# Kernel tuning notes

Measured on AMD Instinct MI355X. Metric: run time of the kernel, lower is better.

The kernel has to match this reference:

```python
import jax, jax.numpy as jnp
import numpy as np

B, S, D, H = 4, 2048, 1024, 16
NEG = -1e10  # matches the module's -10000000000.0 additive mask


def setup_inputs() -> dict:
    key = jax.random.key(0)
    k1, k2, k3, k4, k5 = jax.random.split(key, 5)
    scale = 0.02
    return {
        "x": jax.random.normal(k1, (B, S, D), dtype=jnp.float32),
        "w_qkv": jax.random.normal(k2, (D, 3 * D), dtype=jnp.float32) * scale,
        "b_qkv": jax.random.normal(k3, (3 * D,), dtype=jnp.float32) * scale,
        "w_out": jax.random.normal(k4, (D, D), dtype=jnp.float32) * scale,
        "b_out": jax.random.normal(k5, (D,), dtype=jnp.float32) * scale,
    }


def reference(x, w_qkv, b_qkv, w_out, b_out):
    b, s, d = x.shape
    hd = d // H  # per-head dim
    qkv = x @ w_qkv + b_qkv  # [b,s,3d]
    qq, kk, vv = jnp.split(qkv, 3, axis=-1)
    # [b,h,s,hd]
    qq = qq.reshape(b, s, H, hd).transpose(0, 2, 1, 3)
    kk = kk.reshape(b, s, H, hd).transpose(0, 2, 1, 3)
    vv = vv.reshape(b, s, H, hd).transpose(0, 2, 1, 3)
    scale = 1.0 / float(hd) ** 0.5
    # additive causal mask: NEG above diagonal, 0 on/below (as in module)
    mask = (1.0 - jnp.tri(s, dtype=jnp.float32)) * NEG
    attn = jnp.einsum("bhqd,bhkd->bhqk", qq, kk) * scale + mask
    attn = jax.nn.softmax(attn, axis=-1)
    out = jnp.einsum("bhqk,bhkd->bhqd", attn, vv)  # [b,h,s,hd]
    out = out.transpose(0, 2, 1, 3).reshape(b, s, d)
    return out @ w_out + b_out
```

## Files before the change

### kernel.cpp

```cpp
#include <hip/hip_runtime.h>
#include <hip/hip_bf16.h>
#include <stdint.h>
#include <type_traits>


#define B_   4
#define S_   2048
#define D_   1024
#define H_   16
#define HD_  64
#define MTOK (B_ * S_)
#define BK   32
#define QSCALE 0.18033688011112042f

typedef __attribute__((ext_vector_type(8))) short bfx8;
typedef __attribute__((ext_vector_type(4))) float fx4;
typedef __attribute__((ext_vector_type(16))) float fx16;

#define MAX3(a,b,c) fmaxf(fmaxf(a,b),c)

static __device__ __forceinline__ unsigned short f2bf(float f) {
    union { float f; uint32_t u; } v{f};
    uint32_t u = v.u;
    u += 0x7fffu + ((u >> 16) & 1u);
    return (unsigned short)(u >> 16);
}

static __device__ __forceinline__ uint32_t cvtpk(float lo, float hi) {
    uint32_t r;
    asm volatile("v_cvt_pk_bf16_f32 %0, %1, %2" : "=v"(r) : "v"(lo), "v"(hi));
    return r;
}

static __device__ __forceinline__ void pswap(uint32_t& a, uint32_t& b) {
    asm volatile("v_permlane32_swap_b32 %0, %1" : "+v"(a), "+v"(b));
}

static __device__ __forceinline__ void gll16(const unsigned short* g, const unsigned short* l) {
    typedef const __attribute__((address_space(1))) void* gp_t;
    typedef __attribute__((address_space(3))) void* lp_t;
    __builtin_amdgcn_global_load_lds((gp_t)(uintptr_t)g, (lp_t)(uint32_t)(uintptr_t)l, 16, 0, 0);
}

__global__ void k_conv_x(const float* __restrict__ x, unsigned short* __restrict__ xb, int n8) {
    int i = blockIdx.x * blockDim.x + threadIdx.x;
    int stride = gridDim.x * blockDim.x;
    for (; i < n8; i += stride) {
        const float4* p = (const float4*)(x + (size_t)i * 8);
        float4 a = p[0], b = p[1];
        bfx8 o;
        o[0]=f2bf(a.x); o[1]=f2bf(a.y); o[2]=f2bf(a.z); o[3]=f2bf(a.w);
        o[4]=f2bf(b.x); o[5]=f2bf(b.y); o[6]=f2bf(b.z); o[7]=f2bf(b.w);
        *(bfx8*)(xb + (size_t)i * 8) = o;
    }
}

__global__ void k_transpose_bf(const float* __restrict__ w, unsigned short* __restrict__ wt,
                               int K, int N) {
    int idx = blockIdx.x * blockDim.x + threadIdx.x;
    int total = N * (K / 8);
    if (idx >= total) return;
    int n  = idx % N;
    int k0 = (idx / N) * 8;
    bfx8 o;
#pragma unroll
    for (int j = 0; j < 8; ++j) o[j] = f2bf(w[(size_t)(k0 + j) * N + n]);
    *(bfx8*)(wt + (size_t)n * K + k0) = o;
}

__global__ void k_transpose_v(const unsigned short* __restrict__ Vw,
                              unsigned short* __restrict__ Vt) {
    __shared__ unsigned short lds[64][72];
    const int bg = blockIdx.x;
    const int bh = bg >> 5;
    const int st = (bg & 31) * 64;
    const int t = threadIdx.x;
#pragma unroll
    for (int j = 0; j < 2; ++j) {
        int c = t + 256 * j;
        int row = c >> 3, q = c & 7;
        *(bfx8*)&lds[row][q * 8] = *(const bfx8*)&Vw[((size_t)bh * S_ + st + row) * HD_ + q * 8];
    }
    __syncthreads();
#pragma unroll
    for (int j = 0; j < 2; ++j) {
        int c = t + 256 * j;
        int d = c >> 3, q = c & 7;
        bfx8 o;
#pragma unroll
        for (int e = 0; e < 8; ++e) o[e] = lds[q * 8 + e][d];
        *(bfx8*)&Vt[((size_t)bh * HD_ + d) * S_ + st + q * 8] = o;
    }
}

__launch_bounds__(256)
__global__ void k_gemm_qkv(const unsigned short* __restrict__ A,
                           const unsigned short* __restrict__ Bt,
                           const float* __restrict__ bias,
                           unsigned short* __restrict__ Qw,
                           unsigned short* __restrict__ Kw,
                           unsigned short* __restrict__ Vw) {
    __shared__ unsigned short Al[2][128 * BK];
    __shared__ unsigned short Bl[2][128 * BK];
    const int wg = blockIdx.x;
    const int lin = (wg & 7) * 192 + (wg >> 3);
    const int ny = lin / 24, nx = lin - ny * 24;
    const int m0 = ny * 128;
    const int n0 = nx * 128;
    const int t = threadIdx.x;
    const int w = t >> 6, l = t & 63;
    const int wr = w >> 1, wc = w & 1;
    const int lr = l & 15, lg = l >> 4;
    const int srow = l >> 2;
    const int scol = (l & 3) * 8;
    fx4 acc[4][4] = {};

    auto stage = [&](int k0, int buf) {
#pragma unroll
        for (int j = 0; j < 2; ++j) {
            int rb = j * 64 + w * 16;
            gll16(&A [(size_t)(m0 + rb + srow) * D_ + k0 + scol], &Al[buf][rb * BK]);
            gll16(&Bt[(size_t)(n0 + rb + srow) * D_ + k0 + scol], &Bl[buf][rb * BK]);
        }
    };
    auto compute = [&](auto bufc) {
        constexpr int BUF = decltype(bufc)::value;
        bfx8 af[4], bf[4];
#pragma unroll
        for (int i = 0; i < 4; ++i) af[i] = *(const bfx8*)&Al[BUF][(wr * 64 + i * 16 + lr) * BK + lg * 8];
#pragma unroll
        for (int i = 0; i < 4; ++i) bf[i] = *(const bfx8*)&Bl[BUF][(wc * 64 + i * 16 + lr) * BK + lg * 8];
#pragma unroll
        for (int mi = 0; mi < 4; ++mi)
#pragma unroll
            for (int ni = 0; ni < 4; ++ni)
                acc[mi][ni] = __builtin_amdgcn_mfma_f32_16x16x32_bf16(bf[ni], af[mi], acc[mi][ni], 0, 0, 0);
    };

    stage(0, 0);
    __syncthreads();
    for (int k0 = 0; k0 < D_; k0 += 2 * BK) {
        if (k0 + BK < D_) stage(k0 + BK, 1);
        compute(std::integral_constant<int, 0>{});
        __syncthreads();
        if (k0 + 2 * BK < D_) stage(k0 + 2 * BK, 0);
        compute(std::integral_constant<int, 1>{});
        __syncthreads();
    }

#pragma unroll
    for (int ni = 0; ni < 4; ++ni) {
        const int nn = n0 + wc * 64 + ni * 16 + lg * 4;
        const int mat = nn >> 10;
        const int h = (nn & 1023) >> 6, dd = nn & 63;
        const float4 bv = *(const float4*)&bias[nn];
        unsigned short* dst = (mat == 0) ? Qw : (mat == 1) ? Kw : Vw;
        const float sc = (mat == 0) ? QSCALE : 1.0f;
#pragma unroll
        for (int mi = 0; mi < 4; ++mi) {
            const int m = m0 + wr * 64 + mi * 16 + lr;
            const int b = m >> 11, s = m & 2047;
            const int bh = b * H_ + h;
            fx4 v = acc[mi][ni];
            float o0 = (v[0] + bv.x) * sc, o1 = (v[1] + bv.y) * sc;
            float o2 = (v[2] + bv.z) * sc, o3 = (v[3] + bv.w) * sc;
            uint2 u; u.x = cvtpk(o0, o1); u.y = cvtpk(o2, o3);
            *(uint2*)&dst[((size_t)bh * S_ + s) * HD_ + dd] = u;
        }
    }
}

__launch_bounds__(512, 4)
__global__ void k_attn(const unsigned short* __restrict__ Qw,
                       const unsigned short* __restrict__ Kw,
                       const unsigned short* __restrict__ Vt,
                       unsigned short* __restrict__ Ob) {
    __shared__ unsigned short Sh[4][64 * 64];
    const int wg = blockIdx.x;
    const int xcd = wg & 7, ix = wg >> 3;
    const int bh = xcd * 8 + (ix >> 3);
    const int pi = ix & 7;
    const int t = threadIdx.x;
    const int w = t >> 6, l = t & 63;
    const int lq = l & 31, hi = l >> 5;
    const int tile = (w < 4) ? (15 - pi) : pi;
    const int qr = tile * 128 + (w & 3) * 32;
    const int NT = 32 - 2 * pi;

    const unsigned short* Qp = Qw + (size_t)bh * S_ * HD_;
    const unsigned short* Kp = Kw + (size_t)bh * S_ * HD_;
    const unsigned short* Vp = Vt + (size_t)bh * HD_ * S_;

    bfx8 qf[4];
#pragma unroll
    for (int kb = 0; kb < 4; ++kb)
        qf[kb] = *(const bfx8*)&Qp[(size_t)(qr + lq) * HD_ + kb * 16 + hi * 8];

    fx16 oacc[2] = {};
    float mrow = -1e30f, lsum = 0.f;

    const int sid0 = t, sid1 = t + 512;
    const int srow0 = (sid0 & 511) >> 3, sq0 = sid0 & 7;
    const int srow1 = (sid1 & 511) >> 3, sq1 = sid1 & 7;
    const int soff0 = srow0 * 128 + ((sq0 * 16) ^ ((srow0 & 7) << 4));
    const int soff1 = srow1 * 128 + ((sq1 * 16) ^ ((srow1 & 7) << 4));

    auto step = [&](auto bufc, int tkv) {
        constexpr int BUF = decltype(bufc)::value;
        const int kv0 = tkv * 64;
        const bool pre = (tkv + 1 < NT);
        bfx8 sreg0, sreg1;
        if (pre) {
            const int kn = kv0 + 64;
            sreg0 = *(const bfx8*)&Kp[(size_t)(kn + srow0) * HD_ + sq0 * 8];
            sreg1 = *(const bfx8*)&Vp[(size_t)srow1 * S_ + kn + sq1 * 8];
        }
        if (kv0 <= qr + 31) {
            const char* Kb = (const char*)&Sh[BUF][0];
            const char* Vb = (const char*)&Sh[2 + BUF][0];
            const int sw = (lq & 7) << 4;
            fx16 s0 = {}, s1 = {};
            __builtin_amdgcn_s_setprio(1);
#pragma unroll
            for (int kb = 0; kb < 4; ++kb) {
                const int cb = kb * 32 + hi * 16;
                bfx8 k0 = *(const bfx8*)(Kb + lq * 128 + (cb ^ sw));
                bfx8 k1 = *(const bfx8*)(Kb + (32 + lq) * 128 + (cb ^ sw));
                s0 = __builtin_amdgcn_mfma_f32_32x32x16_bf16(k0, qf[kb], s0, 0, 0, 0);
                s1 = __builtin_amdgcn_mfma_f32_32x32x16_bf16(k1, qf[kb], s1, 0, 0, 0);
            }
            __builtin_amdgcn_s_setprio(0);
            if (kv0 + 63 > qr) {
                const int qrel = qr + lq - kv0;
#pragma unroll
                for (int r = 0; r < 16; ++r) {
                    const int kvo = (r & 3) + 8 * (r >> 2) + 4 * hi;
                    if (kvo > qrel)      s0[r] = -1e30f;
                    if (kvo + 32 > qrel) s1[r] = -1e30f;
                }
            }
            float a0 = MAX3(s0[0], s0[1], s0[2]);
            float a1 = MAX3(s0[3], s0[4], s0[5]);
            float a2 = MAX3(s0[6], s0[7], s0[8]);
            float a3 = MAX3(s0[9], s0[10], s0[11]);
            float a4 = MAX3(s0[12], s0[13], s0[14]);
            float a5 = MAX3(s0[15], s1[0], s1[1]);
            float a6 = MAX3(s1[2], s1[3], s1[4]);
            float a7 = MAX3(s1[5], s1[6], s1[7]);
            float a8 = MAX3(s1[8], s1[9], s1[10]);
            float a9 = MAX3(s1[11], s1[12], s1[13]);
            float aA = fmaxf(s1[14], s1[15]);
            float b0 = MAX3(a0, a1, a2);
            float b1 = MAX3(a3, a4, a5);
            float b2 = MAX3(a6, a7, a8);
            float b3 = fmaxf(a9, aA);
            float mx = MAX3(fmaxf(b0, b1), b2, b3);
            mx = fmaxf(mx, __shfl_xor(mx, 32));
            if (!__all(mx <= mrow + 8.f)) {
                const float mnew = fmaxf(mrow, mx);
                const float al = exp2f(mrow - mnew);
                mrow = mnew;
#pragma unroll
                for (int r = 0; r < 16; ++r) { oacc[0][r] *= al; oacc[1][r] *= al; }
                lsum *= al;
            }
            uint32_t pk0[8], pk1[8];
            float ps = 0.f;
#pragma unroll
            for (int j = 0; j < 8; ++j) {
                float p0 = exp2f(s0[2 * j] - mrow), p1 = exp2f(s0[2 * j + 1] - mrow);
                float p2 = exp2f(s1[2 * j] - mrow), p3 = exp2f(s1[2 * j + 1] - mrow);
                ps += (p0 + p1) + (p2 + p3);
                pk0[j] = cvtpk(p0, p1);
                pk1[j] = cvtpk(p2, p3);
            }
            lsum += ps + __shfl_xor(ps, 32);
            __builtin_amdgcn_s_setprio(1);
#pragma unroll
            for (int sl = 0; sl < 4; ++sl) {
                const uint32_t* pk = (sl < 2) ? pk0 : pk1;
                const int s = sl & 1;
                uint32_t w0 = pk[4 * s], w1 = pk[4 * s + 1], w2 = pk[4 * s + 2], w3 = pk[4 * s + 3];
                pswap(w0, w2);
                pswap(w1, w3);
                union { uint32_t u[4]; bfx8 v; } pf;
                pf.u[0] = w0; pf.u[1] = w1; pf.u[2] = w2; pf.u[3] = w3;
                const int cb = sl * 32 + hi * 16;
                bfx8 v0 = *(const bfx8*)(Vb + lq * 128 + (cb ^ sw));
                bfx8 v1 = *(const bfx8*)(Vb + (32 + lq) * 128 + (cb ^ sw));
                oacc[0] = __builtin_amdgcn_mfma_f32_32x32x16_bf16(v0, pf.v, oacc[0], 0, 0, 0);
                oacc[1] = __builtin_amdgcn_mfma_f32_32x32x16_bf16(v1, pf.v, oacc[1], 0, 0, 0);
            }
            __builtin_amdgcn_s_setprio(0);
        }
        if (pre) {
            *(bfx8*)((char*)&Sh[BUF ^ 1][0] + soff0) = sreg0;
            *(bfx8*)((char*)&Sh[2 + (BUF ^ 1)][0] + soff1) = sreg1;
        }
    };

    {
        bfx8 s0 = *(const bfx8*)&Kp[(size_t)srow0 * HD_ + sq0 * 8];
        bfx8 s1 = *(const bfx8*)&Vp[(size_t)srow1 * S_ + sq1 * 8];
        *(bfx8*)((char*)&Sh[0][0] + soff0) = s0;
        *(bfx8*)((char*)&Sh[2][0] + soff1) = s1;
    }
    __syncthreads();

    for (int tkv = 0; tkv < NT; tkv += 2) {
        step(std::integral_constant<int, 0>{}, tkv);
        __syncthreads();
        step(std::integral_constant<int, 1>{}, tkv + 1);
        __syncthreads();
    }

    const int b = bh >> 4, h = bh & 15;
    const float iv = __builtin_amdgcn_rcpf(lsum);
    unsigned short* orow = Ob + ((size_t)b * S_ + qr + lq) * D_ + h * 64;
#pragma unroll
    for (int db = 0; db < 2; ++db)
#pragma unroll
        for (int rq = 0; rq < 4; ++rq) {
            uint2 u;
            u.x = cvtpk(oacc[db][rq * 4 + 0] * iv, oacc[db][rq * 4 + 1] * iv);
            u.y = cvtpk(oacc[db][rq * 4 + 2] * iv, oacc[db][rq * 4 + 3] * iv);
            *(uint2*)&orow[db * 32 + rq * 8 + hi * 4] = u;
        }
}

__launch_bounds__(256)
__global__ void k_gemm_proj(const unsigned short* __restrict__ A,
                            const unsigned short* __restrict__ Bt,
                            const float* __restrict__ bias,
                            float* __restrict__ out) {
    __shared__ unsigned short Al[2][128 * BK];
    __shared__ unsigned short Bl[2][128 * BK];
    const int wg = blockIdx.x;
    const int lin = (wg & 7) * 64 + (wg >> 3);
    const int ny = lin >> 3, nx = lin & 7;
    const int m0 = ny * 128;
    const int n0 = nx * 128;
    const int t = threadIdx.x;
    const int w = t >> 6, l = t & 63;
    const int wr = w >> 1, wc = w & 1;
    const int lr = l & 15, lg = l >> 4;
    const int srow = l >> 2;
    const int scol = (l & 3) * 8;
    fx4 acc[4][4] = {};

    auto stage = [&](int k0, int buf) {
#pragma unroll
        for (int j = 0; j < 2; ++j) {
            int rb = j * 64 + w * 16;
            gll16(&A [(size_t)(m0 + rb + srow) * D_ + k0 + scol], &Al[buf][rb * BK]);
            gll16(&Bt[(size_t)(n0 + rb + srow) * D_ + k0 + scol], &Bl[buf][rb * BK]);
        }
    };
    auto compute = [&](auto bufc) {
        constexpr int BUF = decltype(bufc)::value;
        bfx8 af[4], bf[4];
#pragma unroll
        for (int i = 0; i < 4; ++i) af[i] = *(const bfx8*)&Al[BUF][(wr * 64 + i * 16 + lr) * BK + lg * 8];
#pragma unroll
        for (int i = 0; i < 4; ++i) bf[i] = *(const bfx8*)&Bl[BUF][(wc * 64 + i * 16 + lr) * BK + lg * 8];
#pragma unroll
        for (int mi = 0; mi < 4; ++mi)
#pragma unroll
            for (int ni = 0; ni < 4; ++ni)
                acc[mi][ni] = __builtin_amdgcn_mfma_f32_16x16x32_bf16(bf[ni], af[mi], acc[mi][ni], 0, 0, 0);
    };

    stage(0, 0);
    __syncthreads();
    for (int k0 = 0; k0 < D_; k0 += 2 * BK) {
        if (k0 + BK < D_) stage(k0 + BK, 1);
        compute(std::integral_constant<int, 0>{});
        __syncthreads();
        if (k0 + 2 * BK < D_) stage(k0 + 2 * BK, 0);
        compute(std::integral_constant<int, 1>{});
        __syncthreads();
    }
#pragma unroll
    for (int ni = 0; ni < 4; ++ni) {
        const int nn = n0 + wc * 64 + ni * 16 + lg * 4;
        const float4 bv = *(const float4*)&bias[nn];
#pragma unroll
        for (int mi = 0; mi < 4; ++mi) {
            const int m = m0 + wr * 64 + mi * 16 + lr;
            fx4 v = acc[mi][ni];
            float4 o; o.x = v[0] + bv.x; o.y = v[1] + bv.y; o.z = v[2] + bv.z; o.w = v[3] + bv.w;
            *(float4*)&out[(size_t)m * D_ + nn] = o;
        }
    }
}

extern "C" void kernel_launch(void* const* d_in, const int* in_sizes, int n_in,
                              void* d_out, int out_size, void* d_ws, size_t ws_size,
                              hipStream_t stream) {
    const float* x     = (const float*)d_in[0];
    const float* w_qkv = (const float*)d_in[1];
    const float* b_qkv = (const float*)d_in[2];
    const float* w_out = (const float*)d_in[3];
    const float* b_out = (const float*)d_in[4];
    float* out = (float*)d_out;

    unsigned short* xb    = (unsigned short*)d_ws;
    unsigned short* wqkvT = xb    + (size_t)MTOK * D_;
    unsigned short* woutT = wqkvT + (size_t)3 * D_ * D_;
    unsigned short* Qw    = woutT + (size_t)D_ * D_;
    unsigned short* Kw    = Qw    + (size_t)MTOK * D_;
    unsigned short* Vw    = Kw    + (size_t)MTOK * D_;
    unsigned short* attnb = Vw    + (size_t)MTOK * D_;
    unsigned short* Vt    = xb;

    k_conv_x<<<2048, 256, 0, stream>>>(x, xb, MTOK * D_ / 8);
    k_transpose_bf<<<(3 * D_ * (D_ / 8)) / 256, 256, 0, stream>>>(w_qkv, wqkvT, D_, 3 * D_);
    k_transpose_bf<<<(D_ * (D_ / 8)) / 256, 256, 0, stream>>>(w_out, woutT, D_, D_);
    k_gemm_qkv<<<1536, 256, 0, stream>>>(xb, wqkvT, b_qkv, Qw, Kw, Vw);
    k_transpose_v<<<2048, 256, 0, stream>>>(Vw, Vt);
    k_attn<<<512, 512, 0, stream>>>(Qw, Kw, Vt, attnb);
    k_gemm_proj<<<512, 256, 0, stream>>>(attnb, woutT, b_out, out);
}
```

Before: 204.8 us.

## Rewrite QKV GEMM with 256x256 tiles, swizzled LDS and interleaved staging

The QKV projection GEMM moves from 128x128 tiles with BK=32 and 256 threads to 256x256 tiles with BK=64 and 512 threads (8 waves, each computing 128x64). LDS rows are XOR-swizzled to avoid bank conflicts. Global-to-LDS prefetch of the next k-tile is split into four quarters interleaved between MFMA quadrants, using explicit vmcnt waits, barriers and setprio. The aim is higher arithmetic intensity and better overlap of loads with MFMA, at the cost of more registers and LDS per block and only 384 blocks to fill the CUs.

```diff
diff --git a/kernel.cpp b/kernel.cpp
--- a/kernel.cpp
+++ b/kernel.cpp
@@ -11,6 +11,8 @@
 #define HD_  64
 #define MTOK (B_ * S_)
 #define BK   32
+#define QBM  256
+#define QBK  64
 #define QSCALE 0.18033688011112042f
 
 typedef __attribute__((ext_vector_type(8))) short bfx8;
@@ -93,78 +95,129 @@
     }
 }
 
-__launch_bounds__(256)
+__launch_bounds__(512, 2)
 __global__ void k_gemm_qkv(const unsigned short* __restrict__ A,
                            const unsigned short* __restrict__ Bt,
                            const float* __restrict__ bias,
                            unsigned short* __restrict__ Qw,
                            unsigned short* __restrict__ Kw,
                            unsigned short* __restrict__ Vw) {
-    __shared__ unsigned short Al[2][128 * BK];
-    __shared__ unsigned short Bl[2][128 * BK];
+    __shared__ unsigned short Al[2][QBM * QBK];
+    __shared__ unsigned short Bl[2][QBM * QBK];
     const int wg = blockIdx.x;
-    const int lin = (wg & 7) * 192 + (wg >> 3);
-    const int ny = lin / 24, nx = lin - ny * 24;
-    const int m0 = ny * 128;
-    const int n0 = nx * 128;
+    const int lin = (wg & 7) * 48 + (wg >> 3);
+    const int ny = lin / 12, nx = lin - ny * 12;
+    const int m0 = ny * QBM, n0 = nx * QBM;
     const int t = threadIdx.x;
     const int w = t >> 6, l = t & 63;
-    const int wr = w >> 1, wc = w & 1;
+    const int wr = w >> 2, wc = w & 3;
     const int lr = l & 15, lg = l >> 4;
-    const int srow = l >> 2;
-    const int scol = (l & 3) * 8;
-    fx4 acc[4][4] = {};
-
-    auto stage = [&](int k0, int buf) {
+    const int sw = (lr & 7) << 4;
+
+    fx4 acc[8][4] = {};
+    bfx8 afH[4][2], bf0[2][2], bf1[2][2];
+
+    const int g_r  = l >> 3;
+    const int g_cb = ((l & 7) * 16) ^ (g_r << 4);
+
+    auto stage_half = [&](int buf, int kt1, int half) {
+        const int k0 = kt1 * QBK;
+        const int gr0 = (half >> 1) * 128;
 #pragma unroll
         for (int j = 0; j < 2; ++j) {
-            int rb = j * 64 + w * 16;
-            gll16(&A [(size_t)(m0 + rb + srow) * D_ + k0 + scol], &Al[buf][rb * BK]);
-            gll16(&Bt[(size_t)(n0 + rb + srow) * D_ + k0 + scol], &Bl[buf][rb * BK]);
-        }
-    };
-    auto compute = [&](auto bufc) {
-        constexpr int BUF = decltype(bufc)::value;
-        bfx8 af[4], bf[4];
-#pragma unroll
-        for (int i = 0; i < 4; ++i) af[i] = *(const bfx8*)&Al[BUF][(wr * 64 + i * 16 + lr) * BK + lg * 8];
-#pragma unroll
-        for (int i = 0; i < 4; ++i) bf[i] = *(const bfx8*)&Bl[BUF][(wc * 64 + i * 16 + lr) * BK + lg * 8];
+            const int rbase = gr0 + j * 64 + w * 8;
+            const int grow = rbase + g_r;
+            if (half & 1)
+                gll16(&Bt[(size_t)(n0 + grow) * D_ + k0] + (g_cb >> 1), &Bl[buf][rbase * QBK]);
+            else
+                gll16(&A [(size_t)(m0 + grow) * D_ + k0] + (g_cb >> 1), &Al[buf][rbase * QBK]);
+        }
+    };
+
+    auto loadA = [&](const unsigned short* base, int mh) {
+        const char* p = (const char*)base;
+#pragma unroll
+        for (int mi = 0; mi < 4; ++mi) {
+            const int row = wr * 128 + mh * 64 + mi * 16 + lr;
+#pragma unroll
+            for (int kk = 0; kk < 2; ++kk)
+                afH[mi][kk] = *(const bfx8*)(p + row * 128 + ((kk * 64 + lg * 16) ^ sw));
+        }
+    };
+    auto loadB = [&](const unsigned short* base, int nh, bfx8 (*bf)[2]) {
+        const char* p = (const char*)base;
+#pragma unroll
+        for (int ni = 0; ni < 2; ++ni) {
+            const int row = wc * 64 + nh * 32 + ni * 16 + lr;
+#pragma unroll
+            for (int kk = 0; kk < 2; ++kk)
+                bf[ni][kk] = *(const bfx8*)(p + row * 128 + ((kk * 64 + lg * 16) ^ sw));
+        }
+    };
+    auto quad = [&](int mh, int nh, bfx8 (*bf)[2]) {
+        __builtin_amdgcn_s_setprio(1);
 #pragma unroll
         for (int mi = 0; mi < 4; ++mi)
 #pragma unroll
-            for (int ni = 0; ni < 4; ++ni)
-                acc[mi][ni] = __builtin_amdgcn_mfma_f32_16x16x32_bf16(bf[ni], af[mi], acc[mi][ni], 0, 0, 0);
-    };
-
-    stage(0, 0);
-    __syncthreads();
-    for (int k0 = 0; k0 < D_; k0 += 2 * BK) {
-        if (k0 + BK < D_) stage(k0 + BK, 1);
-        compute(std::integral_constant<int, 0>{});
-        __syncthreads();
-        if (k0 + 2 * BK < D_) stage(k0 + 2 * BK, 0);
-        compute(std::integral_constant<int, 1>{});
-        __syncthreads();
-    }
-
+            for (int ni = 0; ni < 2; ++ni)
+#pragma unroll
+                for (int kk = 0; kk < 2; ++kk)
+                    acc[mh * 4 + mi][nh * 2 + ni] = __builtin_amdgcn_mfma_f32_16x16x32_bf16(
+                        bf[ni][kk], afH[mi][kk], acc[mh * 4 + mi][nh * 2 + ni], 0, 0, 0);
+        __builtin_amdgcn_s_setprio(0);
+    };
+
+    stage_half(0, 0, 0); stage_half(0, 0, 1); stage_half(0, 0, 2); stage_half(0, 0, 3);
+
+    const int NKT = D_ / QBK;
+    for (int kt = 0; kt < NKT; ++kt) {
+        const int cur = kt & 1, nxt = cur ^ 1;
+        const bool pre = (kt + 1 < NKT);
+        if (pre) {
+            stage_half(nxt, kt + 1, 0);
+            asm volatile("s_waitcnt vmcnt(2)" ::: "memory");
+        } else {
+            asm volatile("s_waitcnt vmcnt(0)" ::: "memory");
+        }
+        __builtin_amdgcn_sched_barrier(0);
+        __builtin_amdgcn_s_barrier();
+        loadA(&Al[cur][0], 0);
+        loadB(&Bl[cur][0], 0, bf0);
+        quad(0, 0, bf0);
+        __builtin_amdgcn_s_barrier();
+        loadB(&Bl[cur][0], 1, bf1);
+        if (pre) stage_half(nxt, kt + 1, 1);
+        __builtin_amdgcn_s_barrier();
+        quad(0, 1, bf1);
+        __builtin_amdgcn_s_barrier();
+        loadA(&Al[cur][0], 1);
+        if (pre) stage_half(nxt, kt + 1, 2);
+        __builtin_amdgcn_s_barrier();
+        quad(1, 1, bf1);
+        __builtin_amdgcn_s_barrier();
+        if (pre) stage_half(nxt, kt + 1, 3);
+        __builtin_amdgcn_s_barrier();
+        quad(1, 0, bf0);
+        __builtin_amdgcn_s_barrier();
+    }
+
+    const int mat = n0 >> 10;
+    unsigned short* dst = (mat == 0) ? Qw : (mat == 1) ? Kw : Vw;
+    const float sc = (mat == 0) ? QSCALE : 1.0f;
 #pragma unroll
     for (int ni = 0; ni < 4; ++ni) {
         const int nn = n0 + wc * 64 + ni * 16 + lg * 4;
-        const int mat = nn >> 10;
         const int h = (nn & 1023) >> 6, dd = nn & 63;
         const float4 bv = *(const float4*)&bias[nn];
-        unsigned short* dst = (mat == 0) ? Qw : (mat == 1) ? Kw : Vw;
-        const float sc = (mat == 0) ? QSCALE : 1.0f;
-#pragma unroll
-        for (int mi = 0; mi < 4; ++mi) {
-            const int m = m0 + wr * 64 + mi * 16 + lr;
+#pragma unroll
+        for (int mi = 0; mi < 8; ++mi) {
+            const int m = m0 + wr * 128 + mi * 16 + lr;
             const int b = m >> 11, s = m & 2047;
             const int bh = b * H_ + h;
             fx4 v = acc[mi][ni];
-            float o0 = (v[0] + bv.x) * sc, o1 = (v[1] + bv.y) * sc;
-            float o2 = (v[2] + bv.z) * sc, o3 = (v[3] + bv.w) * sc;
-            uint2 u; u.x = cvtpk(o0, o1); u.y = cvtpk(o2, o3);
+            uint2 u;
+            u.x = cvtpk((v[0] + bv.x) * sc, (v[1] + bv.y) * sc);
+            u.y = cvtpk((v[2] + bv.z) * sc, (v[3] + bv.w) * sc);
             *(uint2*)&dst[((size_t)bh * S_ + s) * HD_ + dd] = u;
         }
     }
@@ -416,7 +469,7 @@
     k_conv_x<<<2048, 256, 0, stream>>>(x, xb, MTOK * D_ / 8);
     k_transpose_bf<<<(3 * D_ * (D_ / 8)) / 256, 256, 0, stream>>>(w_qkv, wqkvT, D_, 3 * D_);
     k_transpose_bf<<<(D_ * (D_ / 8)) / 256, 256, 0, stream>>>(w_out, woutT, D_, D_);
-    k_gemm_qkv<<<1536, 256, 0, stream>>>(xb, wqkvT, b_qkv, Qw, Kw, Vw);
+    k_gemm_qkv<<<384, 512, 0, stream>>>(xb, wqkvT, b_qkv, Qw, Kw, Vw);
     k_transpose_v<<<2048, 256, 0, stream>>>(Vw, Vt);
     k_attn<<<512, 512, 0, stream>>>(Qw, Kw, Vt, attnb);
     k_gemm_proj<<<512, 256, 0, stream>>>(attnb, woutT, b_out, out);
```

Result: faster. 198.1 us (-3.3%).

## Split attention into 256-thread single-tile blocks and drop QKV GEMM double buffering

Applied to the files above, without the earlier changes.

The attention kernel drops its paired heavy/light causal tiles in 512-thread blocks and launches 1024 blocks of 256 threads, each covering one 128-row query tile. Blocks are ordered heaviest first, and each thread now stages two K and two V chunks. Separately, the QKV GEMM loses its double-buffered LDS pipeline and becomes single-buffered with two barriers per K step, halving LDS use. The GEMM change exposes global-load latency. The attention change gives up the explicit load balancing, which now depends on scheduling order.

```diff
diff --git a/kernel.cpp b/kernel.cpp
--- a/kernel.cpp
+++ b/kernel.cpp
@@ -100,8 +100,8 @@
                            unsigned short* __restrict__ Qw,
                            unsigned short* __restrict__ Kw,
                            unsigned short* __restrict__ Vw) {
-    __shared__ unsigned short Al[2][128 * BK];
-    __shared__ unsigned short Bl[2][128 * BK];
+    __shared__ unsigned short Al[128 * BK];
+    __shared__ unsigned short Bl[128 * BK];
     const int wg = blockIdx.x;
     const int lin = (wg & 7) * 192 + (wg >> 3);
     const int ny = lin / 24, nx = lin - ny * 24;
@@ -115,37 +115,25 @@
     const int scol = (l & 3) * 8;
     fx4 acc[4][4] = {};
 
-    auto stage = [&](int k0, int buf) {
+    for (int k0 = 0; k0 < D_; k0 += BK) {
+        __syncthreads();
 #pragma unroll
         for (int j = 0; j < 2; ++j) {
             int rb = j * 64 + w * 16;
-            gll16(&A [(size_t)(m0 + rb + srow) * D_ + k0 + scol], &Al[buf][rb * BK]);
-            gll16(&Bt[(size_t)(n0 + rb + srow) * D_ + k0 + scol], &Bl[buf][rb * BK]);
-        }
-    };
-    auto compute = [&](auto bufc) {
-        constexpr int BUF = decltype(bufc)::value;
+            gll16(&A [(size_t)(m0 + rb + srow) * D_ + k0 + scol], &Al[rb * BK]);
+            gll16(&Bt[(size_t)(n0 + rb + srow) * D_ + k0 + scol], &Bl[rb * BK]);
+        }
+        __syncthreads();
         bfx8 af[4], bf[4];
 #pragma unroll
-        for (int i = 0; i < 4; ++i) af[i] = *(const bfx8*)&Al[BUF][(wr * 64 + i * 16 + lr) * BK + lg * 8];
-#pragma unroll
-        for (int i = 0; i < 4; ++i) bf[i] = *(const bfx8*)&Bl[BUF][(wc * 64 + i * 16 + lr) * BK + lg * 8];
+        for (int i = 0; i < 4; ++i) af[i] = *(const bfx8*)&Al[(wr * 64 + i * 16 + lr) * BK + lg * 8];
+#pragma unroll
+        for (int i = 0; i < 4; ++i) bf[i] = *(const bfx8*)&Bl[(wc * 64 + i * 16 + lr) * BK + lg * 8];
 #pragma unroll
         for (int mi = 0; mi < 4; ++mi)
 #pragma unroll
             for (int ni = 0; ni < 4; ++ni)
                 acc[mi][ni] = __builtin_amdgcn_mfma_f32_16x16x32_bf16(bf[ni], af[mi], acc[mi][ni], 0, 0, 0);
-    };
-
-    stage(0, 0);
-    __syncthreads();
-    for (int k0 = 0; k0 < D_; k0 += 2 * BK) {
-        if (k0 + BK < D_) stage(k0 + BK, 1);
-        compute(std::integral_constant<int, 0>{});
-        __syncthreads();
-        if (k0 + 2 * BK < D_) stage(k0 + 2 * BK, 0);
-        compute(std::integral_constant<int, 1>{});
-        __syncthreads();
     }
 
 #pragma unroll
@@ -170,7 +158,7 @@
     }
 }
 
-__launch_bounds__(512, 4)
+__launch_bounds__(256, 4)
 __global__ void k_attn(const unsigned short* __restrict__ Qw,
                        const unsigned short* __restrict__ Kw,
                        const unsigned short* __restrict__ Vt,
@@ -178,14 +166,13 @@
     __shared__ unsigned short Sh[4][64 * 64];
     const int wg = blockIdx.x;
     const int xcd = wg & 7, ix = wg >> 3;
-    const int bh = xcd * 8 + (ix >> 3);
-    const int pi = ix & 7;
+    const int bh = xcd * 8 + (ix >> 4);
+    const int ti = 15 - (ix & 15);
     const int t = threadIdx.x;
     const int w = t >> 6, l = t & 63;
     const int lq = l & 31, hi = l >> 5;
-    const int tile = (w < 4) ? (15 - pi) : pi;
-    const int qr = tile * 128 + (w & 3) * 32;
-    const int NT = 32 - 2 * pi;
+    const int qr = ti * 128 + w * 32;
+    const int NT = 2 * ti + 2;
 
     const unsigned short* Qp = Qw + (size_t)bh * S_ * HD_;
     const unsigned short* Kp = Kw + (size_t)bh * S_ * HD_;
@@ -199,21 +186,22 @@
     fx16 oacc[2] = {};
     float mrow = -1e30f, lsum = 0.f;
 
-    const int sid0 = t, sid1 = t + 512;
-    const int srow0 = (sid0 & 511) >> 3, sq0 = sid0 & 7;
-    const int srow1 = (sid1 & 511) >> 3, sq1 = sid1 & 7;
-    const int soff0 = srow0 * 128 + ((sq0 * 16) ^ ((srow0 & 7) << 4));
-    const int soff1 = srow1 * 128 + ((sq1 * 16) ^ ((srow1 & 7) << 4));
+    const int sr0 = t >> 3,         sq0 = t & 7;
+    const int sr1 = (t + 256) >> 3, sq1 = (t + 256) & 7;
+    const int so0 = sr0 * 128 + ((sq0 * 16) ^ ((sr0 & 7) << 4));
+    const int so1 = sr1 * 128 + ((sq1 * 16) ^ ((sr1 & 7) << 4));
 
     auto step = [&](auto bufc, int tkv) {
         constexpr int BUF = decltype(bufc)::value;
         const int kv0 = tkv * 64;
         const bool pre = (tkv + 1 < NT);
-        bfx8 sreg0, sreg1;
+        bfx8 sK0, sK1, sV0, sV1;
         if (pre) {
             const int kn = kv0 + 64;
-            sreg0 = *(const bfx8*)&Kp[(size_t)(kn + srow0) * HD_ + sq0 * 8];
-            sreg1 = *(const bfx8*)&Vp[(size_t)srow1 * S_ + kn + sq1 * 8];
+            sK0 = *(const bfx8*)&Kp[(size_t)(kn + sr0) * HD_ + sq0 * 8];
+            sK1 = *(const bfx8*)&Kp[(size_t)(kn + sr1) * HD_ + sq1 * 8];
+            sV0 = *(const bfx8*)&Vp[(size_t)sr0 * S_ + kn + sq0 * 8];
+            sV1 = *(const bfx8*)&Vp[(size_t)sr1 * S_ + kn + sq1 * 8];
         }
         if (kv0 <= qr + 31) {
             const char* Kb = (const char*)&Sh[BUF][0];
@@ -294,16 +282,22 @@
             __builtin_amdgcn_s_setprio(0);
         }
         if (pre) {
-            *(bfx8*)((char*)&Sh[BUF ^ 1][0] + soff0) = sreg0;
-            *(bfx8*)((char*)&Sh[2 + (BUF ^ 1)][0] + soff1) = sreg1;
+            *(bfx8*)((char*)&Sh[BUF ^ 1][0] + so0) = sK0;
+            *(bfx8*)((char*)&Sh[BUF ^ 1][0] + so1) = sK1;
+            *(bfx8*)((char*)&Sh[2 + (BUF ^ 1)][0] + so0) = sV0;
+            *(bfx8*)((char*)&Sh[2 + (BUF ^ 1)][0] + so1) = sV1;
         }
     };
 
     {
-        bfx8 s0 = *(const bfx8*)&Kp[(size_t)srow0 * HD_ + sq0 * 8];
-        bfx8 s1 = *(const bfx8*)&Vp[(size_t)srow1 * S_ + sq1 * 8];
-        *(bfx8*)((char*)&Sh[0][0] + soff0) = s0;
-        *(bfx8*)((char*)&Sh[2][0] + soff1) = s1;
+        bfx8 sK0 = *(const bfx8*)&Kp[(size_t)sr0 * HD_ + sq0 * 8];
+        bfx8 sK1 = *(const bfx8*)&Kp[(size_t)sr1 * HD_ + sq1 * 8];
+        bfx8 sV0 = *(const bfx8*)&Vp[(size_t)sr0 * S_ + sq0 * 8];
+        bfx8 sV1 = *(const bfx8*)&Vp[(size_t)sr1 * S_ + sq1 * 8];
+        *(bfx8*)((char*)&Sh[0][0] + so0) = sK0;
+        *(bfx8*)((char*)&Sh[0][0] + so1) = sK1;
+        *(bfx8*)((char*)&Sh[2][0] + so0) = sV0;
+        *(bfx8*)((char*)&Sh[2][0] + so1) = sV1;
     }
     __syncthreads();
 
@@ -418,6 +412,6 @@
     k_transpose_bf<<<(D_ * (D_ / 8)) / 256, 256, 0, stream>>>(w_out, woutT, D_, D_);
     k_gemm_qkv<<<1536, 256, 0, stream>>>(xb, wqkvT, b_qkv, Qw, Kw, Vw);
     k_transpose_v<<<2048, 256, 0, stream>>>(Vw, Vt);
-    k_attn<<<512, 512, 0, stream>>>(Qw, Kw, Vt, attnb);
+    k_attn<<<1024, 256, 0, stream>>>(Qw, Kw, Vt, attnb);
     k_gemm_proj<<<512, 256, 0, stream>>>(attnb, woutT, b_out, out);
 }
```

After: 266.9 us. 1.3x slower.
